# Performance work log

Hardware: AMD Instinct MI355X
Metric: run time of the kernel (lower is better)

Reference implementation:

```python
import jax, jax.numpy as jnp
import numpy as np

DIM = 1024
NUM_HEADS = 16
SCALE = DIM ** (-0.5)  # NOTE: source scales by full dim, not head_dim


def setup_inputs() -> dict:
    key = jax.random.key(0)
    ks = jax.random.split(key, 10)
    B, N, C = 2, 2048, DIM
    s = 0.02
    return {
        "x": jax.random.normal(ks[0], (B, N, C), dtype=jnp.float32),
        "queries": jax.random.normal(ks[1], (B, N, C), dtype=jnp.float32),
        "wq": jax.random.normal(ks[2], (C, C), dtype=jnp.float32) * s,
        "bq": jnp.zeros((C,), dtype=jnp.float32),
        "wk": jax.random.normal(ks[3], (C, C), dtype=jnp.float32) * s,
        "bk": jnp.zeros((C,), dtype=jnp.float32),
        "wv": jax.random.normal(ks[4], (C, C), dtype=jnp.float32) * s,
        "bv": jnp.zeros((C,), dtype=jnp.float32),
        "wo": jax.random.normal(ks[5], (C, C), dtype=jnp.float32) * s,
        "bo": jnp.zeros((C,), dtype=jnp.float32),
    }


def reference(x, queries, wq, bq, wk, bk, wv, bv, wo, bo):
    B, N, C = queries.shape
    H = NUM_HEADS
    D = C // H
    # torch Linear: y = x @ W.T + b  (W is [out, in])
    q = (queries @ wq.T + bq).reshape(B, N, H, D).transpose(0, 2, 1, 3)  # [B,H,N,D]
    k = (x @ wk.T + bk).reshape(B, N, H, D).transpose(0, 2, 1, 3)
    v = (x @ wv.T + bv).reshape(B, N, H, D).transpose(0, 2, 1, 3)
    attn = jnp.einsum("bhqd,bhkd->bhqk", q, k) * SCALE  # full-dim scale per source
    attn = jax.nn.softmax(attn, axis=-1)
    out = jnp.einsum("bhqk,bhkd->bhqd", attn, v)  # [B,H,N,D]
    out = out.transpose(0, 2, 1, 3).reshape(B, N, C)
    return out @ wo.T + bo
```

## Files before the change

### kernel.cpp

```cpp
#include <hip/hip_runtime.h>
#include <hip/hip_bf16.h>

typedef __attribute__((ext_vector_type(8))) short bf16x8;
typedef __attribute__((ext_vector_type(4))) float f32x4;
typedef unsigned short u16;
typedef unsigned int u32;

#define MFMA16(a,b,c) __builtin_amdgcn_mfma_f32_16x16x32_bf16((a),(b),(c),0,0,0)

#if defined(__has_builtin) && __has_builtin(__builtin_amdgcn_exp2f)
#define EXP2(x) __builtin_amdgcn_exp2f(x)
#else
#define EXP2(x) exp2f(x)
#endif

#define QSCALE 0.045084220027780106f

__device__ __forceinline__ u16 f2bf(float f) {
  union { float f; unsigned int u; } v; v.f = f;
  unsigned int r = v.u + 0x7FFFu + ((v.u >> 16) & 1u);
  return (u16)(r >> 16);
}

__device__ __forceinline__ u32 pkbf(float a, float b) {
  union { __hip_bfloat162 h; u32 u; } cv;
  cv.h = __float22bfloat162_rn(make_float2(a, b));
  return cv.u;
}

__device__ __forceinline__ void gld16(const void* g, void* l) {
  __builtin_amdgcn_global_load_lds(
      (__attribute__((address_space(1))) void*)(g),
      (__attribute__((address_space(3))) void*)(l), 16, 0, 0);
}

#define SB __builtin_amdgcn_sched_barrier(0);
#define BARR  SB __builtin_amdgcn_s_barrier(); SB

__global__ __launch_bounds__(256) void cast_all(
    const float* __restrict__ x, const float* __restrict__ qu,
    const float* __restrict__ wq, const float* __restrict__ wk,
    const float* __restrict__ wv, const float* __restrict__ wo,
    u16* __restrict__ xb, u16* __restrict__ qub,
    u16* __restrict__ wqb, u16* __restrict__ wkb,
    u16* __restrict__ wvb, u16* __restrict__ wob)
{
  int i = blockIdx.x * 256 + threadIdx.x;
  const float4* src; u16* dst; int off;
  if (i < 1048576)      { src = (const float4*)qu; dst = qub; off = i; }
  else if (i < 2097152) { src = (const float4*)x;  dst = xb;  off = i - 1048576; }
  else if (i < 2359296) { src = (const float4*)wq; dst = wqb; off = i - 2097152; }
  else if (i < 2621440) { src = (const float4*)wk; dst = wkb; off = i - 2359296; }
  else if (i < 2883584) { src = (const float4*)wv; dst = wvb; off = i - 2621440; }
  else                  { src = (const float4*)wo; dst = wob; off = i - 2883584; }
  float4 v = src[off];
  ushort4 r; r.x = f2bf(v.x); r.y = f2bf(v.y); r.z = f2bf(v.z); r.w = f2bf(v.w);
  ((ushort4*)dst)[off] = r;
}

__global__ __launch_bounds__(256) void gemm_qkv(
    const u16* __restrict__ qub, const u16* __restrict__ xb,
    const u16* __restrict__ wqb, const u16* __restrict__ wkb, const u16* __restrict__ wvb,
    const float* __restrict__ bq, const float* __restrict__ bk, const float* __restrict__ bv,
    u16* __restrict__ qhd, u16* __restrict__ khd, u16* __restrict__ vtd)
{
  __shared__ u16 As[2][128 * 64];
  __shared__ u16 Bs[2][128 * 64];
  int tid = threadIdx.x, w = tid >> 6, lane = tid & 63;
  int c = lane & 15, quad = lane >> 4;
  int bm = blockIdx.x, bn = blockIdx.y, z = blockIdx.z;
  int wm = w >> 1, wn = w & 1;
  const u16* A = (z == 0) ? qub : xb;
  const u16* W = (z == 0) ? wqb : (z == 1) ? wkb : wvb;
  f32x4 acc[4][4] = {};

#define QSTAGE(B, K0)                                                           \
  {                                                                             \
    _Pragma("unroll") for (int i = 0; i < 4; i++) {                             \
      int seg = i * 256 + w * 64 + lane;                                        \
      int row = seg >> 3, pseg = seg & 7;                                       \
      int lseg = pseg ^ (row & 7);                                              \
      gld16(A + (size_t)(bm * 128 + row) * 1024 + (K0) + lseg * 8,              \
            &As[B][(i * 256 + w * 64) * 8]);                                    \
      gld16(W + (size_t)(bn * 128 + row) * 1024 + (K0) + lseg * 8,              \
            &Bs[B][(i * 256 + w * 64) * 8]);                                    \
    }                                                                           \
  }

#define QCOMP(PH)                                                               \
  {                                                                             \
    _Pragma("unroll") for (int ks = 0; ks < 2; ks++) {                          \
      bf16x8 af[4], bfr[4];                                                     \
      _Pragma("unroll") for (int mt = 0; mt < 4; mt++) {                        \
        int row = wm * 64 + mt * 16 + c;                                        \
        int cseg = (ks * 4 + quad) ^ (row & 7);                                 \
        af[mt] = *(const bf16x8*)&As[PH][(row * 8 + cseg) * 8];                 \
      }                                                                         \
      _Pragma("unroll") for (int nt = 0; nt < 4; nt++) {                        \
        int row = wn * 64 + nt * 16 + c;                                        \
        int cseg = (ks * 4 + quad) ^ (row & 7);                                 \
        bfr[nt] = *(const bf16x8*)&Bs[PH][(row * 8 + cseg) * 8];                \
      }                                                                         \
      if (z < 2) {                                                              \
        _Pragma("unroll") for (int ct = 0; ct < 4; ct++)                        \
          _Pragma("unroll") for (int tt = 0; tt < 4; tt++)                      \
            acc[ct][tt] = MFMA16(bfr[ct], af[tt], acc[ct][tt]);                 \
      } else {                                                                  \
        _Pragma("unroll") for (int mt = 0; mt < 4; mt++)                        \
          _Pragma("unroll") for (int nt = 0; nt < 4; nt++)                      \
            acc[mt][nt] = MFMA16(af[mt], bfr[nt], acc[mt][nt]);                 \
      }                                                                         \
    }                                                                           \
  }

#define WV8 { SB asm volatile("s_waitcnt vmcnt(8)" ::: "memory"); SB }
#define WV0 { SB asm volatile("s_waitcnt vmcnt(0)" ::: "memory"); SB }

  QSTAGE(0, 0)
  int k0 = 64;
  for (int kk = 0; kk < 7; kk++) {
    BARR QSTAGE(1, k0) WV8 BARR QCOMP(0)
    k0 += 64;
    BARR QSTAGE(0, k0) WV8 BARR QCOMP(1)
    k0 += 64;
  }
  BARR QSTAGE(1, 960) WV8 BARR QCOMP(0)
  BARR WV0 BARR QCOMP(1)
#undef WV0
#undef WV8
#undef QCOMP
#undef QSTAGE

  if (z < 2) {
    const float* bias = (z == 0) ? bq : bk;
    u16* dst = (z == 0) ? qhd : khd;
    float sc = (z == 0) ? QSCALE : 1.0f;
    float4 bbs[4];
#pragma unroll
    for (int ct = 0; ct < 4; ct++) {
      float4 b4 = *(const float4*)&bias[bn * 128 + wn * 64 + ct * 16 + quad * 4];
      bbs[ct].x = b4.x * sc; bbs[ct].y = b4.y * sc;
      bbs[ct].z = b4.z * sc; bbs[ct].w = b4.w * sc;
    }
#pragma unroll
    for (int ct = 0; ct < 4; ct++) {
      int ch = bn * 128 + wn * 64 + ct * 16 + quad * 4;
      int h = ch >> 6, d0 = ch & 63;
#pragma unroll
      for (int tt = 0; tt < 4; tt++) {
        int tok = bm * 128 + wm * 64 + tt * 16 + c;
        int b = tok >> 11, n = tok & 2047;
        float v0 = fmaf(acc[ct][tt][0], sc, bbs[ct].x);
        float v1 = fmaf(acc[ct][tt][1], sc, bbs[ct].y);
        float v2 = fmaf(acc[ct][tt][2], sc, bbs[ct].z);
        float v3 = fmaf(acc[ct][tt][3], sc, bbs[ct].w);
        uint2 pk; pk.x = pkbf(v0, v1); pk.y = pkbf(v2, v3);
        *(uint2*)&dst[((size_t)(b * 16 + h) * 2048 + n) * 64 + d0] = pk;
      }
    }
  } else {
    float bval[4];
#pragma unroll
    for (int nt = 0; nt < 4; nt++)
      bval[nt] = bv[bn * 128 + wn * 64 + nt * 16 + c];
#pragma unroll
    for (int mt = 0; mt < 4; mt++) {
      int tokl = (mt & 2) * 16 + quad * 8 + (mt & 1) * 4;
      int tok = bm * 128 + wm * 64 + tokl;
      int b = tok >> 11, np = tok & 2047;
#pragma unroll
      for (int nt = 0; nt < 4; nt++) {
        int ch = bn * 128 + wn * 64 + nt * 16 + c;
        int h = ch >> 6, d = ch & 63;
        float v0 = acc[mt][nt][0] + bval[nt];
        float v1 = acc[mt][nt][1] + bval[nt];
        float v2 = acc[mt][nt][2] + bval[nt];
        float v3 = acc[mt][nt][3] + bval[nt];
        uint2 pk; pk.x = pkbf(v0, v1); pk.y = pkbf(v2, v3);
        *(uint2*)&vtd[((size_t)(b * 16 + h) * 64 + d) * 2048 + np] = pk;
      }
    }
  }
}

__global__ __launch_bounds__(128, 2) void attn(
    const u16* __restrict__ qh, const u16* __restrict__ kh,
    const u16* __restrict__ vt, u16* __restrict__ ot)
{
  __shared__ u16 KL[2][2][32 * 64];
  __shared__ u16 VL[2][2][64 * 32];
  __shared__ float CL[64];
  int tid = threadIdx.x, w = tid >> 6, lane = tid & 63;
  int c = lane & 15, quad = lane >> 4;
  int bh = blockIdx.x, qt = blockIdx.y;

  const u16* qp = qh + ((size_t)bh * 2048 + qt * 64) * 64;
  bf16x8 Qf[4][2];
#pragma unroll
  for (int q2 = 0; q2 < 4; q2++)
#pragma unroll
    for (int ks = 0; ks < 2; ks++)
      Qf[q2][ks] = *(const bf16x8*)(qp + (size_t)(q2 * 16 + c) * 64 + ks * 32 + quad * 8);

  int kro = lane >> 3;
  int ksw = ((lane & 7) ^ (kro & 7)) * 8;
  const u16* kg = kh + (size_t)bh * 131072 + (size_t)w * 65536 + kro * 64 + ksw;
  int vro = lane >> 2;
  int vsw = ((lane & 3) ^ (vro & 3)) * 8;
  const u16* vg = vt + (size_t)bh * 131072 + (size_t)vro * 2048 + w * 1024 + vsw;

  int off0 = c * 64 + ((quad) ^ (c & 7)) * 8;
  int off1 = c * 64 + ((4 + quad) ^ (c & 7)) * 8;
  int offV = c * 32 + ((quad ^ (c & 3)) & 3) * 8;

#define STAGE(B)                                                                \
  {                                                                             \
    gld16(kg,          &KL[w][B][0]);                                           \
    gld16(kg + 512,    &KL[w][B][512]);                                         \
    gld16(kg + 1024,   &KL[w][B][1024]);                                        \
    gld16(kg + 1536,   &KL[w][B][1536]);                                        \
    gld16(vg,          &VL[w][B][0]);                                           \
    gld16(vg + 32768,  &VL[w][B][512]);                                         \
    gld16(vg + 65536,  &VL[w][B][1024]);                                        \
    gld16(vg + 98304,  &VL[w][B][1536]);                                        \
    kg += 2048; vg += 32;                                                       \
  }

  f32x4 O[4][4] = {};
  f32x4 Lacc[4] = {};
  bf16x8 vone;
#pragma unroll
  for (int j = 0; j < 8; j++) vone[j] = (short)0x3F80;

#define ITER(PH, PREF)                                                          \
  {                                                                             \
    asm volatile("s_waitcnt lgkmcnt(0)" ::: "memory");                          \
    __builtin_amdgcn_sched_barrier(0);                                          \
    if (PREF) STAGE(PH ^ 1)                                                     \
    if (PREF) { asm volatile("s_waitcnt vmcnt(8)" ::: "memory"); }              \
    else      { asm volatile("s_waitcnt vmcnt(0)" ::: "memory"); }              \
    __builtin_amdgcn_sched_barrier(0);                                          \
    const u16* Ks = KL[w][PH];                                                  \
    const u16* Vs = VL[w][PH];                                                  \
    bf16x8 Kf[2][2];                                                            \
    Kf[0][0] = *(const bf16x8*)&Ks[off0];                                       \
    Kf[0][1] = *(const bf16x8*)&Ks[off1];                                       \
    Kf[1][0] = *(const bf16x8*)&Ks[off0 + 1024];                                \
    Kf[1][1] = *(const bf16x8*)&Ks[off1 + 1024];                                \
    f32x4 S[4][2] = {};                                                         \
    _Pragma("unroll") for (int q2 = 0; q2 < 4; q2++)                            \
      _Pragma("unroll") for (int nt = 0; nt < 2; nt++) {                        \
        S[q2][nt] = MFMA16(Kf[nt][0], Qf[q2][0], S[q2][nt]);                    \
        S[q2][nt] = MFMA16(Kf[nt][1], Qf[q2][1], S[q2][nt]);                    \
      }                                                                         \
    bf16x8 pa[4];                                                               \
    _Pragma("unroll") for (int q2 = 0; q2 < 4; q2++) {                          \
      float e0 = EXP2(S[q2][0][0]), e1 = EXP2(S[q2][0][1]);                     \
      float e2 = EXP2(S[q2][0][2]), e3 = EXP2(S[q2][0][3]);                     \
      float e4 = EXP2(S[q2][1][0]), e5 = EXP2(S[q2][1][1]);                     \
      float e6 = EXP2(S[q2][1][2]), e7 = EXP2(S[q2][1][3]);                     \
      union { uint4 u; bf16x8 v; } cv;                                          \
      cv.u.x = pkbf(e0, e1); cv.u.y = pkbf(e2, e3);                             \
      cv.u.z = pkbf(e4, e5); cv.u.w = pkbf(e6, e7);                             \
      pa[q2] = cv.v;                                                            \
    }                                                                           \
    bf16x8 Vf[4];                                                               \
    Vf[0] = *(const bf16x8*)&Vs[offV];                                          \
    Vf[1] = *(const bf16x8*)&Vs[offV + 512];                                    \
    Vf[2] = *(const bf16x8*)&Vs[offV + 1024];                                   \
    Vf[3] = *(const bf16x8*)&Vs[offV + 1536];                                   \
    Lacc[0] = MFMA16(pa[0], vone, Lacc[0]);                                     \
    Lacc[1] = MFMA16(pa[1], vone, Lacc[1]);                                     \
    Lacc[2] = MFMA16(pa[2], vone, Lacc[2]);                                     \
    Lacc[3] = MFMA16(pa[3], vone, Lacc[3]);                                     \
    _Pragma("unroll") for (int q2 = 0; q2 < 4; q2++)                            \
      _Pragma("unroll") for (int dt = 0; dt < 4; dt++)                          \
        O[q2][dt] = MFMA16(pa[q2], Vf[dt], O[q2][dt]);                          \
  }

  STAGE(0)
  for (int t2 = 0; t2 < 15; t2++) {
    ITER(0, 1)
    ITER(1, 1)
  }
  ITER(0, 1)
  ITER(1, 0)
#undef ITER
#undef STAGE

  __syncthreads();
  float* CmbO = (float*)&KL[0][0][0];
  if (w == 1) {
#pragma unroll
    for (int q2 = 0; q2 < 4; q2++) {
      if (c == 0)
        *(f32x4*)&CL[q2 * 16 + quad * 4] = Lacc[q2];
#pragma unroll
      for (int dt = 0; dt < 4; dt++)
#pragma unroll
        for (int j = 0; j < 4; j++)
          CmbO[(q2 * 16 + quad * 4 + j) * 64 + dt * 16 + c] = O[q2][dt][j];
    }
  }
  __syncthreads();
  if (w == 0) {
    int b_ = bh >> 4, h = bh & 15;
#pragma unroll
    for (int q2 = 0; q2 < 4; q2++) {
#pragma unroll
      for (int j = 0; j < 4; j++) {
        int qrow = q2 * 16 + quad * 4 + j;
        float ltot = Lacc[q2][j] + CL[qrow];
        float linv = 1.0f / ltot;
        int n = qt * 64 + qrow;
        u16* op = ot + (((size_t)b_ * 2048 + n) * 16 + h) * 64;
#pragma unroll
        for (int dt = 0; dt < 4; dt++) {
          float o = O[q2][dt][j] + CmbO[qrow * 64 + dt * 16 + c];
          op[dt * 16 + c] = f2bf(o * linv);
        }
      }
    }
  }
}

__global__ __launch_bounds__(256) void gemm_out(
    const u16* __restrict__ Aot, const u16* __restrict__ wob,
    const float* __restrict__ bo, float* __restrict__ out)
{
  __shared__ u16 As[2][64 * 64];
  __shared__ u16 Bs[2][128 * 64];
  int tid = threadIdx.x, w = tid >> 6, lane = tid & 63;
  int bm = blockIdx.x, bn = blockIdx.y;
  int wm = w >> 1, wn = w & 1;
  f32x4 acc[2][4] = {};

#define OSTAGE(B, K0)                                                           \
  {                                                                             \
    _Pragma("unroll") for (int i = 0; i < 2; i++) {                             \
      int seg = i * 256 + tid;                                                  \
      int row = seg >> 3, pseg = seg & 7;                                       \
      int lseg = pseg ^ (row & 7);                                              \
      gld16(Aot + (size_t)(bm * 64 + row) * 1024 + (K0) + lseg * 8,             \
            &As[B][(i * 256 + tid) * 8]);                                       \
    }                                                                           \
    _Pragma("unroll") for (int i = 0; i < 4; i++) {                             \
      int seg = i * 256 + tid;                                                  \
      int row = seg >> 3, pseg = seg & 7;                                       \
      int lseg = pseg ^ (row & 7);                                              \
      gld16(wob + (size_t)(bn * 128 + row) * 1024 + (K0) + lseg * 8,            \
            &Bs[B][(i * 256 + tid) * 8]);                                       \
    }                                                                           \
  }

#define OCOMP(PH)                                                               \
  {                                                                             \
    _Pragma("unroll") for (int ks = 0; ks < 2; ks++) {                          \
      bf16x8 af[2], bfr[4];                                                     \
      _Pragma("unroll") for (int mt = 0; mt < 2; mt++) {                        \
        int row = wm * 32 + mt * 16 + (lane & 15);                              \
        int cseg = (ks * 4 + (lane >> 4)) ^ (row & 7);                          \
        af[mt] = *(const bf16x8*)&As[PH][(row * 8 + cseg) * 8];                 \
      }                                                                         \
      _Pragma("unroll") for (int nt = 0; nt < 4; nt++) {                        \
        int row = wn * 64 + nt * 16 + (lane & 15);                              \
        int cseg = (ks * 4 + (lane >> 4)) ^ (row & 7);                          \
        bfr[nt] = *(const bf16x8*)&Bs[PH][(row * 8 + cseg) * 8];                \
      }                                                                         \
      _Pragma("unroll") for (int mt = 0; mt < 2; mt++)                          \
        _Pragma("unroll") for (int nt = 0; nt < 4; nt++)                        \
          acc[mt][nt] = MFMA16(af[mt], bfr[nt], acc[mt][nt]);                   \
    }                                                                           \
  }

#define WV6 { SB asm volatile("s_waitcnt vmcnt(6)" ::: "memory"); SB }
#define WV0 { SB asm volatile("s_waitcnt vmcnt(0)" ::: "memory"); SB }

  OSTAGE(0, 0)
  int k0 = 64;
  for (int kk = 0; kk < 7; kk++) {
    BARR OSTAGE(1, k0) WV6 BARR OCOMP(0)
    k0 += 64;
    BARR OSTAGE(0, k0) WV6 BARR OCOMP(1)
    k0 += 64;
  }
  BARR OSTAGE(1, 960) WV6 BARR OCOMP(0)
  BARR WV0 BARR OCOMP(1)
#undef WV0
#undef WV6
#undef OCOMP
#undef OSTAGE

#pragma unroll
  for (int nt = 0; nt < 4; nt++) {
    int o = bn * 128 + wn * 64 + nt * 16 + (lane & 15);
    float bval = bo[o];
#pragma unroll
    for (int mt = 0; mt < 2; mt++)
#pragma unroll
      for (int j = 0; j < 4; j++) {
        int m = bm * 64 + wm * 32 + mt * 16 + (lane >> 4) * 4 + j;
        out[(size_t)m * 1024 + o] = acc[mt][nt][j] + bval;
      }
  }
}

extern "C" void kernel_launch(void* const* d_in, const int* in_sizes, int n_in,
                              void* d_out, int out_size, void* d_ws, size_t ws_size,
                              hipStream_t stream)
{
  const float* x  = (const float*)d_in[0];
  const float* qu = (const float*)d_in[1];
  const float* wq = (const float*)d_in[2];
  const float* bq = (const float*)d_in[3];
  const float* wk = (const float*)d_in[4];
  const float* bk = (const float*)d_in[5];
  const float* wv = (const float*)d_in[6];
  const float* bv = (const float*)d_in[7];
  const float* wo = (const float*)d_in[8];
  const float* bo = (const float*)d_in[9];
  float* out = (float*)d_out;
  char* ws = (char*)d_ws;
  u16* xb  = (u16*)(ws + (size_t)0);
  u16* qub = (u16*)(ws + ((size_t)8  << 20));
  u16* wqb = (u16*)(ws + ((size_t)16 << 20));
  u16* wkb = (u16*)(ws + ((size_t)18 << 20));
  u16* wvb = (u16*)(ws + ((size_t)20 << 20));
  u16* wob = (u16*)(ws + ((size_t)22 << 20));
  u16* qhd = (u16*)(ws + ((size_t)24 << 20));
  u16* khd = (u16*)(ws + ((size_t)32 << 20));
  u16* vtd = (u16*)(ws + ((size_t)40 << 20));
  u16* otd = (u16*)(ws + ((size_t)48 << 20));

  cast_all<<<12288, 256, 0, stream>>>(x, qu, wq, wk, wv, wo,
                                      xb, qub, wqb, wkb, wvb, wob);
  gemm_qkv<<<dim3(32, 8, 3), 256, 0, stream>>>(qub, xb, wqb, wkb, wvb,
                                               bq, bk, bv, qhd, khd, vtd);
  attn<<<dim3(32, 32), 128, 0, stream>>>(qhd, khd, vtd, otd);
  gemm_out<<<dim3(64, 8), 256, 0, stream>>>(otd, wob, bo, out);
}
```

Measured before the change: 202.5 us.

## Fuse fp32-to-bf16 casts into GEMM loads with register-staged pipelining

Removes the separate cast_all kernel and has the QKV and output GEMMs load fp32 inputs and weights directly. They convert to bf16 in registers and write to a single LDS buffer, and the next tile's global loads are prefetched into registers while the current tile is computed. This removes a full read-and-write pass over the activations and weights and one kernel launch. In exchange, each GEMM reads twice the bytes per tile, uses more registers, and drops the async global_load_lds double buffering. Weights are now re-cast by every block that reads them.

```diff
diff --git a/kernel.cpp b/kernel.cpp
--- a/kernel.cpp
+++ b/kernel.cpp
@@ -35,71 +35,66 @@
 }
 
 #define SB __builtin_amdgcn_sched_barrier(0);
-#define BARR  SB __builtin_amdgcn_s_barrier(); SB
-
-__global__ __launch_bounds__(256) void cast_all(
-    const float* __restrict__ x, const float* __restrict__ qu,
+
+__global__ __launch_bounds__(256) void gemm_qkv(
+    const float* __restrict__ qu, const float* __restrict__ x,
     const float* __restrict__ wq, const float* __restrict__ wk,
-    const float* __restrict__ wv, const float* __restrict__ wo,
-    u16* __restrict__ xb, u16* __restrict__ qub,
-    u16* __restrict__ wqb, u16* __restrict__ wkb,
-    u16* __restrict__ wvb, u16* __restrict__ wob)
-{
-  int i = blockIdx.x * 256 + threadIdx.x;
-  const float4* src; u16* dst; int off;
-  if (i < 1048576)      { src = (const float4*)qu; dst = qub; off = i; }
-  else if (i < 2097152) { src = (const float4*)x;  dst = xb;  off = i - 1048576; }
-  else if (i < 2359296) { src = (const float4*)wq; dst = wqb; off = i - 2097152; }
-  else if (i < 2621440) { src = (const float4*)wk; dst = wkb; off = i - 2359296; }
-  else if (i < 2883584) { src = (const float4*)wv; dst = wvb; off = i - 2621440; }
-  else                  { src = (const float4*)wo; dst = wob; off = i - 2883584; }
-  float4 v = src[off];
-  ushort4 r; r.x = f2bf(v.x); r.y = f2bf(v.y); r.z = f2bf(v.z); r.w = f2bf(v.w);
-  ((ushort4*)dst)[off] = r;
-}
-
-__global__ __launch_bounds__(256) void gemm_qkv(
-    const u16* __restrict__ qub, const u16* __restrict__ xb,
-    const u16* __restrict__ wqb, const u16* __restrict__ wkb, const u16* __restrict__ wvb,
-    const float* __restrict__ bq, const float* __restrict__ bk, const float* __restrict__ bv,
+    const float* __restrict__ wv,
+    const float* __restrict__ bq, const float* __restrict__ bk,
+    const float* __restrict__ bv,
     u16* __restrict__ qhd, u16* __restrict__ khd, u16* __restrict__ vtd)
 {
-  __shared__ u16 As[2][128 * 64];
-  __shared__ u16 Bs[2][128 * 64];
+  __shared__ u16 As[128 * 64];
+  __shared__ u16 Bs[128 * 64];
   int tid = threadIdx.x, w = tid >> 6, lane = tid & 63;
   int c = lane & 15, quad = lane >> 4;
   int bm = blockIdx.x, bn = blockIdx.y, z = blockIdx.z;
   int wm = w >> 1, wn = w & 1;
-  const u16* A = (z == 0) ? qub : xb;
-  const u16* W = (z == 0) ? wqb : (z == 1) ? wkb : wvb;
+  const float* A = (z == 0) ? qu : x;
+  const float* W = (z == 0) ? wq : (z == 1) ? wk : wv;
   f32x4 acc[4][4] = {};
-
-#define QSTAGE(B, K0)                                                           \
+  float4 ra[4][2], rb[4][2];
+
+#define QLOAD(K0)                                                               \
   {                                                                             \
     _Pragma("unroll") for (int i = 0; i < 4; i++) {                             \
       int seg = i * 256 + w * 64 + lane;                                        \
       int row = seg >> 3, pseg = seg & 7;                                       \
       int lseg = pseg ^ (row & 7);                                              \
-      gld16(A + (size_t)(bm * 128 + row) * 1024 + (K0) + lseg * 8,              \
-            &As[B][(i * 256 + w * 64) * 8]);                                    \
-      gld16(W + (size_t)(bn * 128 + row) * 1024 + (K0) + lseg * 8,              \
-            &Bs[B][(i * 256 + w * 64) * 8]);                                    \
-    }                                                                           \
-  }
-
-#define QCOMP(PH)                                                               \
+      const float* pa = A + (size_t)(bm * 128 + row) * 1024 + (K0) + lseg * 8;  \
+      const float* pb = W + (size_t)(bn * 128 + row) * 1024 + (K0) + lseg * 8;  \
+      ra[i][0] = *(const float4*)pa; ra[i][1] = *(const float4*)(pa + 4);       \
+      rb[i][0] = *(const float4*)pb; rb[i][1] = *(const float4*)(pb + 4);       \
+    }                                                                           \
+  }
+
+#define QWRITE                                                                  \
+  {                                                                             \
+    _Pragma("unroll") for (int i = 0; i < 4; i++) {                             \
+      int seg = i * 256 + w * 64 + lane;                                        \
+      uint4 wa, wb;                                                             \
+      wa.x = pkbf(ra[i][0].x, ra[i][0].y); wa.y = pkbf(ra[i][0].z, ra[i][0].w); \
+      wa.z = pkbf(ra[i][1].x, ra[i][1].y); wa.w = pkbf(ra[i][1].z, ra[i][1].w); \
+      wb.x = pkbf(rb[i][0].x, rb[i][0].y); wb.y = pkbf(rb[i][0].z, rb[i][0].w); \
+      wb.z = pkbf(rb[i][1].x, rb[i][1].y); wb.w = pkbf(rb[i][1].z, rb[i][1].w); \
+      *(uint4*)&As[seg * 8] = wa;                                               \
+      *(uint4*)&Bs[seg * 8] = wb;                                               \
+    }                                                                           \
+  }
+
+#define QCOMP                                                                   \
   {                                                                             \
     _Pragma("unroll") for (int ks = 0; ks < 2; ks++) {                          \
       bf16x8 af[4], bfr[4];                                                     \
       _Pragma("unroll") for (int mt = 0; mt < 4; mt++) {                        \
         int row = wm * 64 + mt * 16 + c;                                        \
         int cseg = (ks * 4 + quad) ^ (row & 7);                                 \
-        af[mt] = *(const bf16x8*)&As[PH][(row * 8 + cseg) * 8];                 \
+        af[mt] = *(const bf16x8*)&As[(row * 8 + cseg) * 8];                     \
       }                                                                         \
       _Pragma("unroll") for (int nt = 0; nt < 4; nt++) {                        \
         int row = wn * 64 + nt * 16 + c;                                        \
         int cseg = (ks * 4 + quad) ^ (row & 7);                                 \
-        bfr[nt] = *(const bf16x8*)&Bs[PH][(row * 8 + cseg) * 8];                \
+        bfr[nt] = *(const bf16x8*)&Bs[(row * 8 + cseg) * 8];                    \
       }                                                                         \
       if (z < 2) {                                                              \
         _Pragma("unroll") for (int ct = 0; ct < 4; ct++)                        \
@@ -113,23 +108,18 @@
     }                                                                           \
   }
 
-#define WV8 { SB asm volatile("s_waitcnt vmcnt(8)" ::: "memory"); SB }
-#define WV0 { SB asm volatile("s_waitcnt vmcnt(0)" ::: "memory"); SB }
-
-  QSTAGE(0, 0)
-  int k0 = 64;
-  for (int kk = 0; kk < 7; kk++) {
-    BARR QSTAGE(1, k0) WV8 BARR QCOMP(0)
-    k0 += 64;
-    BARR QSTAGE(0, k0) WV8 BARR QCOMP(1)
-    k0 += 64;
-  }
-  BARR QSTAGE(1, 960) WV8 BARR QCOMP(0)
-  BARR WV0 BARR QCOMP(1)
-#undef WV0
-#undef WV8
+  QLOAD(0)
+  for (int st = 0; st < 16; st++) {
+    QWRITE
+    if (st < 15) QLOAD((st + 1) * 64)
+    SB asm volatile("s_waitcnt lgkmcnt(0)" ::: "memory"); SB
+    __builtin_amdgcn_s_barrier(); SB
+    QCOMP
+    SB __builtin_amdgcn_s_barrier(); SB
+  }
 #undef QCOMP
-#undef QSTAGE
+#undef QWRITE
+#undef QLOAD
 
   if (z < 2) {
     const float* bias = (z == 0) ? bq : bk;
@@ -325,47 +315,63 @@
 }
 
 __global__ __launch_bounds__(256) void gemm_out(
-    const u16* __restrict__ Aot, const u16* __restrict__ wob,
+    const u16* __restrict__ Aot, const float* __restrict__ wo,
     const float* __restrict__ bo, float* __restrict__ out)
 {
-  __shared__ u16 As[2][64 * 64];
-  __shared__ u16 Bs[2][128 * 64];
+  __shared__ u16 As[64 * 64];
+  __shared__ u16 Bs[128 * 64];
   int tid = threadIdx.x, w = tid >> 6, lane = tid & 63;
   int bm = blockIdx.x, bn = blockIdx.y;
   int wm = w >> 1, wn = w & 1;
   f32x4 acc[2][4] = {};
-
-#define OSTAGE(B, K0)                                                           \
+  uint4 rA[2];
+  float4 rb[4][2];
+
+#define OLOAD(K0)                                                               \
   {                                                                             \
     _Pragma("unroll") for (int i = 0; i < 2; i++) {                             \
       int seg = i * 256 + tid;                                                  \
       int row = seg >> 3, pseg = seg & 7;                                       \
       int lseg = pseg ^ (row & 7);                                              \
-      gld16(Aot + (size_t)(bm * 64 + row) * 1024 + (K0) + lseg * 8,             \
-            &As[B][(i * 256 + tid) * 8]);                                       \
+      rA[i] = *(const uint4*)(Aot + (size_t)(bm * 64 + row) * 1024 + (K0) + lseg * 8); \
     }                                                                           \
     _Pragma("unroll") for (int i = 0; i < 4; i++) {                             \
       int seg = i * 256 + tid;                                                  \
       int row = seg >> 3, pseg = seg & 7;                                       \
       int lseg = pseg ^ (row & 7);                                              \
-      gld16(wob + (size_t)(bn * 128 + row) * 1024 + (K0) + lseg * 8,            \
-            &Bs[B][(i * 256 + tid) * 8]);                                       \
-    }                                                                           \
-  }
-
-#define OCOMP(PH)                                                               \
+      const float* pb = wo + (size_t)(bn * 128 + row) * 1024 + (K0) + lseg * 8; \
+      rb[i][0] = *(const float4*)pb; rb[i][1] = *(const float4*)(pb + 4);       \
+    }                                                                           \
+  }
+
+#define OWRITE                                                                  \
+  {                                                                             \
+    _Pragma("unroll") for (int i = 0; i < 2; i++) {                             \
+      int seg = i * 256 + tid;                                                  \
+      *(uint4*)&As[seg * 8] = rA[i];                                            \
+    }                                                                           \
+    _Pragma("unroll") for (int i = 0; i < 4; i++) {                             \
+      int seg = i * 256 + tid;                                                  \
+      uint4 wb;                                                                 \
+      wb.x = pkbf(rb[i][0].x, rb[i][0].y); wb.y = pkbf(rb[i][0].z, rb[i][0].w); \
+      wb.z = pkbf(rb[i][1].x, rb[i][1].y); wb.w = pkbf(rb[i][1].z, rb[i][1].w); \
+      *(uint4*)&Bs[seg * 8] = wb;                                               \
+    }                                                                           \
+  }
+
+#define OCOMP                                                                   \
   {                                                                             \
     _Pragma("unroll") for (int ks = 0; ks < 2; ks++) {                          \
       bf16x8 af[2], bfr[4];                                                     \
       _Pragma("unroll") for (int mt = 0; mt < 2; mt++) {                        \
         int row = wm * 32 + mt * 16 + (lane & 15);                              \
         int cseg = (ks * 4 + (lane >> 4)) ^ (row & 7);                          \
-        af[mt] = *(const bf16x8*)&As[PH][(row * 8 + cseg) * 8];                 \
+        af[mt] = *(const bf16x8*)&As[(row * 8 + cseg) * 8];                     \
       }                                                                         \
       _Pragma("unroll") for (int nt = 0; nt < 4; nt++) {                        \
         int row = wn * 64 + nt * 16 + (lane & 15);                              \
         int cseg = (ks * 4 + (lane >> 4)) ^ (row & 7);                          \
-        bfr[nt] = *(const bf16x8*)&Bs[PH][(row * 8 + cseg) * 8];                \
+        bfr[nt] = *(const bf16x8*)&Bs[(row * 8 + cseg) * 8];                    \
       }                                                                         \
       _Pragma("unroll") for (int mt = 0; mt < 2; mt++)                          \
         _Pragma("unroll") for (int nt = 0; nt < 4; nt++)                        \
@@ -373,23 +379,18 @@
     }                                                                           \
   }
 
-#define WV6 { SB asm volatile("s_waitcnt vmcnt(6)" ::: "memory"); SB }
-#define WV0 { SB asm volatile("s_waitcnt vmcnt(0)" ::: "memory"); SB }
-
-  OSTAGE(0, 0)
-  int k0 = 64;
-  for (int kk = 0; kk < 7; kk++) {
-    BARR OSTAGE(1, k0) WV6 BARR OCOMP(0)
-    k0 += 64;
-    BARR OSTAGE(0, k0) WV6 BARR OCOMP(1)
-    k0 += 64;
-  }
-  BARR OSTAGE(1, 960) WV6 BARR OCOMP(0)
-  BARR WV0 BARR OCOMP(1)
-#undef WV0
-#undef WV6
+  OLOAD(0)
+  for (int st = 0; st < 16; st++) {
+    OWRITE
+    if (st < 15) OLOAD((st + 1) * 64)
+    SB asm volatile("s_waitcnt lgkmcnt(0)" ::: "memory"); SB
+    __builtin_amdgcn_s_barrier(); SB
+    OCOMP
+    SB __builtin_amdgcn_s_barrier(); SB
+  }
 #undef OCOMP
-#undef OSTAGE
+#undef OWRITE
+#undef OLOAD
 
 #pragma unroll
   for (int nt = 0; nt < 4; nt++) {
@@ -421,21 +422,13 @@
   const float* bo = (const float*)d_in[9];
   float* out = (float*)d_out;
   char* ws = (char*)d_ws;
-  u16* xb  = (u16*)(ws + (size_t)0);
-  u16* qub = (u16*)(ws + ((size_t)8  << 20));
-  u16* wqb = (u16*)(ws + ((size_t)16 << 20));
-  u16* wkb = (u16*)(ws + ((size_t)18 << 20));
-  u16* wvb = (u16*)(ws + ((size_t)20 << 20));
-  u16* wob = (u16*)(ws + ((size_t)22 << 20));
-  u16* qhd = (u16*)(ws + ((size_t)24 << 20));
-  u16* khd = (u16*)(ws + ((size_t)32 << 20));
-  u16* vtd = (u16*)(ws + ((size_t)40 << 20));
-  u16* otd = (u16*)(ws + ((size_t)48 << 20));
-
-  cast_all<<<12288, 256, 0, stream>>>(x, qu, wq, wk, wv, wo,
-                                      xb, qub, wqb, wkb, wvb, wob);
-  gemm_qkv<<<dim3(32, 8, 3), 256, 0, stream>>>(qub, xb, wqb, wkb, wvb,
+  u16* qhd = (u16*)(ws + (size_t)0);
+  u16* khd = (u16*)(ws + ((size_t)8  << 20));
+  u16* vtd = (u16*)(ws + ((size_t)16 << 20));
+  u16* otd = (u16*)(ws + ((size_t)24 << 20));
+
+  gemm_qkv<<<dim3(32, 8, 3), 256, 0, stream>>>(qu, x, wq, wk, wv,
                                                bq, bk, bv, qhd, khd, vtd);
   attn<<<dim3(32, 32), 128, 0, stream>>>(qhd, khd, vtd, otd);
-  gemm_out<<<dim3(64, 8), 256, 0, stream>>>(otd, wob, bo, out);
-}
+  gemm_out<<<dim3(64, 8), 256, 0, stream>>>(otd, wo, bo, out);
+}
```

Result: slower. 221.7 us (+9.5%).
